# Kernel optimization log

Measured on AMD Instinct MI355X. Metric: run time of the kernel, lower is better.

The kernel has to match this reference:

```python
import jax, jax.numpy as jnp
import numpy as np

B, H, W, C = 16, 48, 48, 256
D_INNER = 2 * C          # ssm_ratio = 2.0
D_STATE = 1
DT_RANK = C // 16        # mamba convention: dt_rank = d_model // 16
HID = 4 * C              # mlp_ratio = 4.0
N = H * W


def _grid_neighbors(h, w):
    idx = np.arange(h * w).reshape(h, w)
    pad_r = -np.ones((1, w), np.int64)
    pad_c = -np.ones((h, 1), np.int64)
    up = np.concatenate([pad_r, idx[:-1]], 0)
    down = np.concatenate([idx[1:], pad_r], 0)
    left = np.concatenate([pad_c, idx[:, :-1]], 1)
    right = np.concatenate([idx[:, 1:], pad_c], 1)
    nb = np.stack([up, down, left, right], -1).reshape(h * w, 4)
    valid = nb >= 0
    return jnp.asarray(np.where(valid, nb, 0), np.int32), jnp.asarray(valid)

_NBR, _VALID = _grid_neighbors(H, W)


def _mst(x):
    """Input-adaptive MST (Prim) on the 4-connected pixel grid.
    Edge weight = exp(1 - cosine_similarity) between adjacent pixel features.
    Returns (order, par): Prim insertion order (a valid BFS-like topological order:
    every node's parent appears earlier) and parent node id per node."""
    b = x.shape[0]
    f = x.reshape(b, N, C)
    f = f / (jnp.linalg.norm(f, axis=-1, keepdims=True) + 1e-8)
    cos = jnp.einsum('bnc,bnkc->bnk', f, f[:, _NBR])          # (B,N,4)
    wgt = jnp.where(_VALID, jnp.exp(1.0 - cos), jnp.inf)

    def prim(wb):
        key = jnp.full((N,), jnp.inf, wb.dtype).at[0].set(0.0)
        par = jnp.zeros((N,), jnp.int32)
        intree = jnp.zeros((N,), bool)

        def step(carry, _):
            key, par, intree = carry
            u = jnp.argmin(jnp.where(intree, jnp.inf, key)).astype(jnp.int32)
            intree = intree.at[u].set(True)
            nb, wv = _NBR[u], wb[u]
            better = (~intree[nb]) & (wv < key[nb])
            key = key.at[nb].set(jnp.where(better, wv, key[nb]))
            par = par.at[nb].set(jnp.where(better, u, par[nb]))
            return (key, par, intree), u

        (_, par, _), order = jax.lax.scan(step, (key, par, intree), None, length=N)
        return order, par

    return jax.vmap(prim)(wgt)


def _ln(x, g, b):
    m = jnp.mean(x, -1, keepdims=True)
    v = jnp.var(x, -1, keepdims=True)
    return (x - m) * jax.lax.rsqrt(v + 1e-5) * g + b


def _tree_ssm(xn, order, par, W_in, b_in, W_xp, W_dt, b_dt, A_log, Dp, W_out, b_out):
    """Mamba-style selective scan generalized to a tree: the hidden state of node v
    recurses from its MST parent instead of the previous sequence position."""
    b = xn.shape[0]
    xf = xn.reshape(b, N, C)
    xz = xf @ W_in + b_in                               # (B,N,2*D_INNER)
    xi, z = xz[..., :D_INNER], xz[..., D_INNER:]
    xi = jax.nn.silu(xi)
    dbc = xi @ W_xp                                     # (B,N,DT_RANK+2)
    dtr = dbc[..., :DT_RANK]
    Bv = dbc[..., DT_RANK:DT_RANK + 1]                  # d_state = 1
    Cv = dbc[..., DT_RANK + 1:DT_RANK + 2]
    dt = jax.nn.softplus(dtr @ W_dt + b_dt)             # (B,N,D_INNER)
    A = -jnp.exp(A_log)                                 # (D_INNER,)
    decay = jnp.exp(dt * A)
    Bx = dt * Bv * xi

    def tree_scan(ob, pb, db, xb):
        def step(hbuf, v):
            hv = db[v] * hbuf[pb[v]] + xb[v]            # h[v] = decay*h[parent] + B*x
            return hbuf.at[v].set(hv), None
        hbuf, _ = jax.lax.scan(step, jnp.zeros((N, D_INNER), db.dtype), ob)
        return hbuf

    h = jax.vmap(tree_scan)(order, par, decay, Bx)      # (B,N,D_INNER)
    y = Cv * h + Dp * xi
    return ((y * jax.nn.silu(z)) @ W_out + b_out).reshape(xn.shape)


def setup_inputs():
    key = jax.random.key(0)
    ks = jax.random.split(key, 8)
    g = lambda k, shp, s=0.02: jax.random.normal(k, shp, jnp.float32) * s
    return {
        "x": jax.random.normal(ks[0], (B, H, W, C), jnp.float32),
        "norm1_w": jnp.ones((C,), jnp.float32), "norm1_b": jnp.zeros((C,), jnp.float32),
        "norm2_w": jnp.ones((C,), jnp.float32), "norm2_b": jnp.zeros((C,), jnp.float32),
        "W_in": g(ks[1], (C, 2 * D_INNER)), "b_in": jnp.zeros((2 * D_INNER,), jnp.float32),
        "W_xp": g(ks[2], (D_INNER, DT_RANK + 2 * D_STATE)),
        "W_dt": g(ks[3], (DT_RANK, D_INNER), 0.1), "b_dt": jnp.full((D_INNER,), -2.0, jnp.float32),
        "A_log": jnp.zeros((D_INNER,), jnp.float32), "Dp": jnp.ones((D_INNER,), jnp.float32),
        "W_out": g(ks[4], (D_INNER, C)), "b_out": jnp.zeros((C,), jnp.float32),
        "fc1_w": g(ks[5], (C, HID)), "fc1_b": jnp.zeros((HID,), jnp.float32),
        "fc2_w": g(ks[6], (HID, C)), "fc2_b": jnp.zeros((C,), jnp.float32),
    }


def reference(x, norm1_w, norm1_b, norm2_w, norm2_b, W_in, b_in, W_xp, W_dt, b_dt,
              A_log, Dp, W_out, b_out, fc1_w, fc1_b, fc2_w, fc2_b):
    order, par = _mst(jax.lax.stop_gradient(x))         # torch.no_grad() MST
    x = x + _tree_ssm(_ln(x, norm1_w, norm1_b), order, par,
                      W_in, b_in, W_xp, W_dt, b_dt, A_log, Dp, W_out, b_out)
    h = jax.nn.gelu(_ln(x, norm2_w, norm2_b) @ fc1_w + fc1_b, approximate=False)
    return x + h @ fc2_w + fc2_b
```

## Files before the change

kernel.cpp:

```cpp
#include <hip/hip_runtime.h>
#include <math.h>

#define NN 2304
#define BB 16
#define CC 256
#define DI 512
#define MM (BB*NN)

typedef __attribute__((ext_vector_type(8))) short bf16x8;
typedef __attribute__((ext_vector_type(4))) float f32x4;

__device__ inline unsigned short f2b(float f){
  unsigned u = __float_as_uint(f);
  u = u + 0x7FFFu + ((u>>16)&1u);
  return (unsigned short)(u>>16);
}
__device__ inline float b2f(unsigned short s){ return __uint_as_float(((unsigned)s)<<16); }
__device__ __forceinline__ int dstep(int d){ return (d==0)?-48:(d==1)?48:(d==2)?-1:1; }

__global__ __launch_bounds__(256) void k_prep(const float* __restrict__ W_in, const float* __restrict__ W_out,
    const float* __restrict__ fc1_w, const float* __restrict__ fc2_w, const float* __restrict__ W_xp,
    unsigned short* __restrict__ WinT, unsigned short* __restrict__ WoutT,
    unsigned short* __restrict__ fc1T, unsigned short* __restrict__ fc2T, float* __restrict__ WxpT)
{
  int idx = blockIdx.x*256 + threadIdx.x;
  if (idx < 262144){ int r=idx>>10, c=idx&1023; WinT[(size_t)c*256 + r] = f2b(W_in[idx]); return; }
  idx -= 262144;
  if (idx < 131072){ int r=idx>>8, c=idx&255; WoutT[(size_t)c*512 + r] = f2b(W_out[idx]); return; }
  idx -= 131072;
  if (idx < 262144){ int r=idx>>10, c=idx&1023; fc1T[(size_t)c*256 + r] = f2b(fc1_w[idx]); return; }
  idx -= 262144;
  if (idx < 262144){ int r=idx>>8, c=idx&255; fc2T[(size_t)c*1024 + r] = f2b(fc2_w[idx]); return; }
  idx -= 262144;
  if (idx < 9216){ int r=idx/18, c=idx-r*18; WxpT[(size_t)c*512 + r] = W_xp[idx]; }
}

__global__ __launch_bounds__(256) void k_normln(const float* __restrict__ xin, const float* __restrict__ g,
    const float* __restrict__ bta, float* __restrict__ innorm, unsigned short* __restrict__ outb)
{
  int row = blockIdx.x*4 + (threadIdx.x>>6); int lane=threadIdx.x&63;
  float4 v = *(const float4*)(xin + (size_t)row*CC + lane*4);
  float sq = v.x*v.x + v.y*v.y + v.z*v.z + v.w*v.w;
  float s  = v.x+v.y+v.z+v.w;
  #pragma unroll
  for (int o=32;o;o>>=1){ sq += __shfl_xor(sq,o); s += __shfl_xor(s,o); }
  if (lane==0) innorm[row] = 1.0f/(sqrtf(sq)+1e-8f);
  float m = s*(1.0f/256.0f);
  float dx=v.x-m, dy=v.y-m, dz=v.z-m, dw=v.w-m;
  float ss=dx*dx+dy*dy+dz*dz+dw*dw;
  #pragma unroll
  for (int o=32;o;o>>=1) ss += __shfl_xor(ss,o);
  float rs = rsqrtf(ss*(1.0f/256.0f)+1e-5f);
  int cb=lane*4;
  unsigned o0 = (unsigned)f2b(dx*rs*g[cb+0]+bta[cb+0]) | ((unsigned)f2b(dy*rs*g[cb+1]+bta[cb+1])<<16);
  unsigned o1 = (unsigned)f2b(dz*rs*g[cb+2]+bta[cb+2]) | ((unsigned)f2b(dw*rs*g[cb+3]+bta[cb+3])<<16);
  *(uint2*)(outb + (size_t)row*CC + cb) = make_uint2(o0,o1);
}

__global__ __launch_bounds__(256) void k_edge(const float* __restrict__ x, const float* __restrict__ innorm, float* __restrict__ wgt){
  int g = blockIdx.x*4 + (threadIdx.x>>6); int lane = threadIdx.x&63;
  int b = g/NN, n = g - b*NN;
  int r = n/48, c = n - (n/48)*48;
  const float* xb = x + ((size_t)b*NN)*CC;
  float4 vu = *(const float4*)(xb + (size_t)n*CC + lane*4);
  int nb0=(r>0)?n-48:-1, nb1=(r<47)?n+48:-1, nb2=(c>0)?n-1:-1, nb3=(c<47)?n+1:-1;
  float d0=0,d1=0,d2=0,d3=0;
  if (nb0>=0){ float4 t=*(const float4*)(xb+(size_t)nb0*CC+lane*4); d0=vu.x*t.x+vu.y*t.y+vu.z*t.z+vu.w*t.w; }
  if (nb1>=0){ float4 t=*(const float4*)(xb+(size_t)nb1*CC+lane*4); d1=vu.x*t.x+vu.y*t.y+vu.z*t.z+vu.w*t.w; }
  if (nb2>=0){ float4 t=*(const float4*)(xb+(size_t)nb2*CC+lane*4); d2=vu.x*t.x+vu.y*t.y+vu.z*t.z+vu.w*t.w; }
  if (nb3>=0){ float4 t=*(const float4*)(xb+(size_t)nb3*CC+lane*4); d3=vu.x*t.x+vu.y*t.y+vu.z*t.z+vu.w*t.w; }
  #pragma unroll
  for (int o=32;o;o>>=1){ d0+=__shfl_xor(d0,o); d1+=__shfl_xor(d1,o); d2+=__shfl_xor(d2,o); d3+=__shfl_xor(d3,o); }
  if (lane==0){
    float inu = innorm[g];
    float inf_ = __uint_as_float(0x7F800000u);
    float4 w;
    w.x = (nb0>=0)? expf(1.0f - d0*(inu*innorm[g-n+nb0])) : inf_;
    w.y = (nb1>=0)? expf(1.0f - d1*(inu*innorm[g-n+nb1])) : inf_;
    w.z = (nb2>=0)? expf(1.0f - d2*(inu*innorm[g-n+nb2])) : inf_;
    w.w = (nb3>=0)? expf(1.0f - d3*(inu*innorm[g-n+nb3])) : inf_;
    *(float4*)(wgt + (size_t)g*4) = w;
  }
}

#define INFB 0x7F800000u
#define NILA 0x3FFFu
__device__ void mst_body(unsigned char* smem, const float* __restrict__ wgt, int b,
    unsigned short* __restrict__ parpos_g, int* __restrict__ lvlorder,
    int* __restrict__ lvlstart, int* __restrict__ nlvl)
{
  unsigned* tmask = (unsigned*)smem;
  unsigned* pk    = (unsigned*)(smem + 9216);
  unsigned* comp   = pk;
  unsigned* bestw  = pk + 2304;
  unsigned* bestid = pk + 4608;
  unsigned short* par   = (unsigned short*)(smem + 46080);
  unsigned short* dpos  = (unsigned short*)(smem + 50688);
  int* hist = (int*)(smem + 55296);
  int* ctr  = (int*)(smem + 64512);
  const int tid = threadIdx.x;
  const float* wb = wgt + (size_t)b*NN*4;

  #pragma unroll
  for (int k=0;k<9;k++){ int v=tid+k*256; comp[v]=v; tmask[v]=0u; }
  __syncthreads();

  for (int round=0; round<14; round++){
    #pragma unroll
    for (int k=0;k<9;k++){ int v=tid+k*256; bestw[v]=INFB; bestid[v]=0xFFFFFFFFu; }
    __syncthreads();
    unsigned candw[9], candi[9];
    #pragma unroll
    for (int k=0;k<9;k++){
      int v=tid+k*256;
      unsigned cv=comp[v];
      int r=v/48, c=v-(v/48)*48;
      float4 w4 = *(const float4*)(wb + (size_t)v*4);
      unsigned cw=INFB, ci=0xFFFFFFFFu;
      if (r>0  && comp[v-48]!=cv){ unsigned wv=__float_as_uint(w4.x); if (wv<cw){cw=wv;ci=(unsigned)(v*4+0);} }
      if (r<47 && comp[v+48]!=cv){ unsigned wv=__float_as_uint(w4.y); if (wv<cw){cw=wv;ci=(unsigned)(v*4+1);} }
      if (c>0  && comp[v-1] !=cv){ unsigned wv=__float_as_uint(w4.z); if (wv<cw){cw=wv;ci=(unsigned)(v*4+2);} }
      if (c<47 && comp[v+1] !=cv){ unsigned wv=__float_as_uint(w4.w); if (wv<cw){cw=wv;ci=(unsigned)(v*4+3);} }
      candw[k]=cw; candi[k]=ci;
      if (cw!=INFB) atomicMin(&bestw[cv], cw);
    }
    __syncthreads();
    #pragma unroll
    for (int k=0;k<9;k++){
      if (candw[k]!=INFB){
        int v=tid+k*256; unsigned cv=comp[v];
        if (bestw[cv]==candw[k]) atomicMin(&bestid[cv], candi[k]);
      }
    }
    __syncthreads();
    unsigned hookS[9];
    int hooked = 0;
    #pragma unroll
    for (int k=0;k<9;k++){
      int v=tid+k*256; hookS[k]=0xFFFFFFFFu;
      if (comp[v]!=(unsigned)v) continue;
      unsigned id=bestid[v];
      if (id==0xFFFFFFFFu) continue;
      int u=(int)(id>>2), d=(int)(id&3);
      int o = u + dstep(d);
      unsigned s = comp[o];
      unsigned sid = bestid[s];
      bool mutual=false;
      if (sid!=0xFFFFFFFFu){
        int su=(int)(sid>>2), sd=(int)(sid&3);
        int so = su + dstep(sd);
        mutual = (comp[so]==(unsigned)v);
      }
      if (!mutual || (unsigned)v>s){ hookS[k]=s; hooked=1; }
    }
    __syncthreads();
    #pragma unroll
    for (int k=0;k<9;k++){
      if (hookS[k]==0xFFFFFFFFu) continue;
      int v=tid+k*256;
      unsigned id=bestid[v];
      int u=(int)(id>>2), d=(int)(id&3);
      int o = u + dstep(d);
      comp[v]=hookS[k];
      atomicOr(&tmask[u], 1u<<d);
      atomicOr(&tmask[o], 1u<<(d^1));
    }
    if (__syncthreads_count(hooked)==0) break;
    for (int it=0; it<16; it++){
      int ch=0;
      #pragma unroll
      for (int k=0;k<9;k++){
        int v=tid+k*256;
        unsigned c1=comp[v], c2=comp[c1];
        if (c1!=c2){ comp[v]=c2; ch=1; }
      }
      if (__syncthreads_count(ch)==0) break;
    }
  }
  __syncthreads();

  int a0;
  { unsigned m0 = tmask[0]; a0 = __ffs((int)(m0&0xFu))-1; }

  for (int pass=0; pass<2; pass++){
    for (int k=0;k<36;k++){
      int a = k*256+tid;
      int v = a>>2, d = a&3;
      unsigned mv = tmask[v];
      unsigned sc = NILA;
      unsigned vl = pass ? 8192u : 0u;
      if ((mv>>d)&1u){
        int w = v + dstep(d);
        unsigned mw = tmask[w];
        int rd = d^1;
        int nd = -1;
        #pragma unroll
        for (int kk=1;kk<=4;kk++){ int c2=(rd+kk)&3; if (nd<0 && ((mw>>c2)&1u)) nd=c2; }
        sc = (unsigned)(w*4+nd);
        if (sc==(unsigned)a0) sc=NILA;
        vl = pass ? (8192u + (((mv>>(4+d))&1u)? 1u : (unsigned)-1)) : 1u;
      }
      pk[a] = (sc<<14) | (vl & 0x3FFFu);
    }
    __syncthreads();
    for (int it=0; it<13; it++){
      unsigned stg[36];
      #pragma unroll
      for (int k=0;k<36;k++){
        int a=k*256+tid;
        unsigned mine=pk[a];
        unsigned s=mine>>14;
        if (s==NILA) stg[k]=mine;
        else {
          unsigned oth=pk[s];
          unsigned nv=(mine&0x3FFFu)+(oth&0x3FFFu);
          if (pass) nv -= 8192u;
          stg[k]=((oth>>14)<<14)|(nv&0x3FFFu);
        }
      }
      __syncthreads();
      #pragma unroll
      for (int k=0;k<36;k++) pk[k*256+tid]=stg[k];
      __syncthreads();
    }
    if (pass==0){
      for (int k=0;k<36;k++){
        int a=k*256+tid;
        int v=a>>2, d=a&3;
        if ((tmask[v]>>d)&1u){
          int w=v+dstep(d);
          int ra=w*4+(d^1);
          if ((pk[a]&0x3FFFu) > (pk[ra]&0x3FFFu)){
            atomicOr(&tmask[v], 16u<<d);
            par[w]=(unsigned short)v;
          }
        }
      }
      __syncthreads();
    }
  }
  if (tid==0){ par[0]=0; dpos[0]=0; ctr[3]=0; }
  __syncthreads();
  for (int k=0;k<36;k++){
    int a=k*256+tid;
    int v=a>>2, d=a&3;
    unsigned mv=tmask[v];
    if (((mv>>d)&1u) && ((mv>>(4+d))&1u)){
      int w=v+dstep(d);
      int S=(int)(pk[a]&0x3FFFu)-8192;
      int dep=1-S;
      dpos[w]=(unsigned short)dep;
      atomicMax(&ctr[3],dep);
    }
  }
  __syncthreads();
  int nlv_=ctr[3]+1;
  for (int i=tid;i<nlv_;i+=256) hist[i]=0;
  __syncthreads();
  for (int i=tid;i<NN;i+=256) atomicAdd(&hist[dpos[i]],1);
  __syncthreads();
  if (tid==0){
    int run=0;
    for (int l=0;l<nlv_;l++){ int c2=hist[l]; hist[l]=run; lvlstart[b*(NN+2)+l]=run; run+=c2; }
    lvlstart[b*(NN+2)+nlv_]=run;
    nlvl[b]=nlv_;
  }
  __syncthreads();
  for (int i=tid;i<NN;i+=256){
    int pos=atomicAdd(&hist[dpos[i]],1);
    lvlorder[b*NN+pos]=i;
    dpos[i]=(unsigned short)pos;
  }
  __syncthreads();
  for (int i=tid;i<NN;i+=256)
    parpos_g[b*NN + dpos[i]] = dpos[par[i]];
}

template<int EPI>
__device__ void gemm_body(unsigned short* lA, unsigned short* lB, int bm, int bn,
    const unsigned short* __restrict__ A, const unsigned short* __restrict__ BT,
    const float* __restrict__ bias, int Ndim, int K,
    const float* __restrict__ addin, float* __restrict__ fout,
    unsigned short* __restrict__ bout0, unsigned short* __restrict__ bout1,
    const int* __restrict__ lvl)
{
  int tid=threadIdx.x, wid=tid>>6, lane=tid&63;
  const unsigned short* Ab = A + (size_t)bm*128*K;
  const unsigned short* Bb = BT + (size_t)bn*128*K;
  int wr=wid>>1, wc=wid&1;
  f32x4 acc[4][4];
  #pragma unroll
  for (int m2=0;m2<4;m2++)
    #pragma unroll
    for (int n2=0;n2<4;n2++)
      #pragma unroll
      for (int j=0;j<4;j++) acc[m2][n2][j]=0.f;
  int r0 = tid>>2, c0 = (tid&3)*8;
  for (int k0=0;k0<K;k0+=32){
    int4 va0 = *(const int4*)(Ab + (size_t)r0*K + k0 + c0);
    int4 va1 = *(const int4*)(Ab + (size_t)(r0+64)*K + k0 + c0);
    int4 vb0 = *(const int4*)(Bb + (size_t)r0*K + k0 + c0);
    int4 vb1 = *(const int4*)(Bb + (size_t)(r0+64)*K + k0 + c0);
    __syncthreads();
    *(int4*)(lA + r0*32 + c0) = va0;
    *(int4*)(lA + (r0+64)*32 + c0) = va1;
    *(int4*)(lB + r0*32 + c0) = vb0;
    *(int4*)(lB + (r0+64)*32 + c0) = vb1;
    __syncthreads();
    int ra = (wr<<6) + (lane&15);
    int rb = (wc<<6) + (lane&15);
    int cb = (lane>>4)<<3;
    bf16x8 af[4], bfr[4];
    #pragma unroll
    for (int m2=0;m2<4;m2++) af[m2] = *(const bf16x8*)(lA + (ra+m2*16)*32 + cb);
    #pragma unroll
    for (int n2=0;n2<4;n2++) bfr[n2] = *(const bf16x8*)(lB + (rb+n2*16)*32 + cb);
    #pragma unroll
    for (int m2=0;m2<4;m2++)
      #pragma unroll
      for (int n2=0;n2<4;n2++)
        acc[m2][n2] = __builtin_amdgcn_mfma_f32_16x16x32_bf16(af[m2], bfr[n2], acc[m2][n2], 0,0,0);
  }
  int rr = (lane>>4)<<2, cc = lane&15;
  #pragma unroll
  for (int m2=0;m2<4;m2++){
    #pragma unroll
    for (int n2=0;n2<4;n2++){
      int col = (bn<<7) + (wc<<6) + (n2<<4) + cc;
      float bs = bias[col];
      #pragma unroll
      for (int j=0;j<4;j++){
        int row = (bm<<7) + (wr<<6) + (m2<<4) + rr + j;
        float v = acc[m2][n2][j] + bs;
        if (EPI==0){
          float sv = v * (1.0f/(1.0f+expf(-v)));
          if (col < DI) bout0[(size_t)row*DI + col] = f2b(sv);
          else          bout1[(size_t)row*DI + col - DI] = f2b(sv);
        } else if (EPI==1){
          size_t oi=(size_t)row*Ndim+col;
          fout[oi] = addin[oi] + v;
        } else if (EPI==2){
          size_t oi=(size_t)row*Ndim+col;
          bout0[oi] = f2b(0.5f*v*(1.0f+erff(v*0.70710678118f)));
        } else if (EPI==3){
          int grow = (row/NN)*NN + lvl[row];
          fout[(size_t)row*Ndim+col] = addin[(size_t)grow*Ndim+col] + v;
        } else {
          int grow = (row/NN)*NN + lvl[row];
          fout[(size_t)grow*Ndim+col] = addin[(size_t)row*Ndim+col] + v;
        }
      }
    }
  }
}

template<int EPI>
__global__ __launch_bounds__(256) void k_gemm(
    const unsigned short* __restrict__ A, const unsigned short* __restrict__ BT,
    const float* __restrict__ bias, int Ndim, int K,
    const float* __restrict__ addin, float* __restrict__ fout,
    unsigned short* __restrict__ bout0, unsigned short* __restrict__ bout1,
    const int* __restrict__ lvl)
{
  __shared__ __align__(16) unsigned short lAB[128*32*2];
  int ntn = Ndim>>7;
  int bm = blockIdx.x/ntn, bn = blockIdx.x - bm*ntn;
  gemm_body<EPI>(lAB, lAB+128*32, bm, bn, A, BT, bias, Ndim, K, addin, fout, bout0, bout1, lvl);
}

__global__ __launch_bounds__(256) void k_fused(
    const unsigned short* __restrict__ xn, const unsigned short* __restrict__ WinT,
    const float* __restrict__ b_in,
    unsigned short* __restrict__ xi_b, unsigned short* __restrict__ sz_b,
    const float* __restrict__ wgt, unsigned short* __restrict__ parpos_g,
    int* __restrict__ lvlorder, int* __restrict__ lvlstart, int* __restrict__ nlvl)
{
  __shared__ __align__(16) unsigned char smem[64528];
  if (blockIdx.x < BB){
    mst_body(smem, wgt, blockIdx.x, parpos_g, lvlorder, lvlstart, nlvl);
  } else {
    int bid = blockIdx.x - BB;
    int bm = bid>>3, bn = bid&7;
    gemm_body<0>((unsigned short*)smem, (unsigned short*)smem + 128*32, bm, bn,
                 xn, WinT, b_in, 1024, 256, nullptr, nullptr, xi_b, sz_b, nullptr);
  }
}

__global__ __launch_bounds__(256) void k_ln(const float* __restrict__ xin, const float* __restrict__ g,
    const float* __restrict__ bta, unsigned short* __restrict__ outb)
{
  int row = blockIdx.x*4 + (threadIdx.x>>6); int lane=threadIdx.x&63;
  float4 v = *(const float4*)(xin + (size_t)row*CC + lane*4);
  float s = v.x+v.y+v.z+v.w;
  #pragma unroll
  for (int o=32;o;o>>=1) s += __shfl_xor(s,o);
  float m = s*(1.0f/256.0f);
  float dx=v.x-m, dy=v.y-m, dz=v.z-m, dw=v.w-m;
  float ss=dx*dx+dy*dy+dz*dz+dw*dw;
  #pragma unroll
  for (int o=32;o;o>>=1) ss += __shfl_xor(ss,o);
  float rs = rsqrtf(ss*(1.0f/256.0f)+1e-5f);
  int cb=lane*4;
  unsigned o0 = (unsigned)f2b(dx*rs*g[cb+0]+bta[cb+0]) | ((unsigned)f2b(dy*rs*g[cb+1]+bta[cb+1])<<16);
  unsigned o1 = (unsigned)f2b(dz*rs*g[cb+2]+bta[cb+2]) | ((unsigned)f2b(dw*rs*g[cb+3]+bta[cb+3])<<16);
  *(uint2*)(outb + (size_t)row*CC + cb) = make_uint2(o0,o1);
}

__global__ __launch_bounds__(256) void k_dbc(const unsigned short* __restrict__ xi_b,
    const float* __restrict__ WxpT, float* __restrict__ dbc)
{
  int row = blockIdx.x*4 + (threadIdx.x>>6); int lane=threadIdx.x&63;
  int4 raw = *(const int4*)(xi_b + (size_t)row*DI + lane*8);
  float xf[8];
  xf[0]=b2f((unsigned short)((unsigned)raw.x&0xFFFFu)); xf[1]=b2f((unsigned short)((unsigned)raw.x>>16));
  xf[2]=b2f((unsigned short)((unsigned)raw.y&0xFFFFu)); xf[3]=b2f((unsigned short)((unsigned)raw.y>>16));
  xf[4]=b2f((unsigned short)((unsigned)raw.z&0xFFFFu)); xf[5]=b2f((unsigned short)((unsigned)raw.z>>16));
  xf[6]=b2f((unsigned short)((unsigned)raw.w&0xFFFFu)); xf[7]=b2f((unsigned short)((unsigned)raw.w>>16));
  for (int jc=0;jc<18;jc++){
    const float* wr_ = WxpT + (size_t)jc*DI + lane*8;
    float s=0.f;
    #pragma unroll
    for (int t=0;t<8;t++) s += xf[t]*wr_[t];
    #pragma unroll
    for (int o=32;o;o>>=1) s += __shfl_xor(s,o);
    if (lane==0) dbc[(size_t)row*18+jc]=s;
  }
}

__global__ __launch_bounds__(512) void k_dbx(const float* __restrict__ dbc, const unsigned short* __restrict__ xi_b,
  const float* __restrict__ W_dt, const float* __restrict__ b_dt, const float* __restrict__ A_log,
  const int* __restrict__ lvlorder,
  unsigned short* __restrict__ dec_cm, unsigned short* __restrict__ bx_cm)
{
  __shared__ int smap[32];
  __shared__ float sd[32][18];
  int c = threadIdx.x;
  int b = blockIdx.x/72, pg = blockIdx.x - b*72;
  int p0 = pg*32;
  if (c<32) smap[c] = b*NN + lvlorder[b*NN + p0 + c];
  __syncthreads();
  for (int i=c;i<32*18;i+=512){ int rr=i/18, q=i-rr*18; sd[rr][q]=dbc[(size_t)smap[rr]*18+q]; }
  __syncthreads();
  float wdt[16];
  #pragma unroll
  for (int r2=0;r2<16;r2++) wdt[r2]=W_dt[r2*DI+c];
  float bd=b_dt[c];
  float nA=-expf(A_log[c]);
  unsigned decp[16], bxp[16];
  #pragma unroll
  for (int rr=0;rr<32;rr++){
    float a=bd;
    #pragma unroll
    for (int r2=0;r2<16;r2++) a += sd[rr][r2]*wdt[r2];
    float dt = (a>20.f)? a : log1pf(expf(a));
    float dec = expf(dt*nA);
    float bx = dt*sd[rr][16]*b2f(xi_b[(size_t)smap[rr]*DI + c]);
    if (rr&1){ decp[rr>>1] |= ((unsigned)f2b(dec))<<16; bxp[rr>>1] |= ((unsigned)f2b(bx))<<16; }
    else     { decp[rr>>1]  =  (unsigned)f2b(dec);      bxp[rr>>1]  =  (unsigned)f2b(bx); }
  }
  size_t chb = ((size_t)b*DI + c)*NN + p0;
  uint4* dp = (uint4*)(dec_cm + chb);
  uint4* bp = (uint4*)(bx_cm + chb);
  #pragma unroll
  for (int q=0;q<4;q++){
    uint4 dv, bv;
    dv.x=decp[q*4+0]; dv.y=decp[q*4+1]; dv.z=decp[q*4+2]; dv.w=decp[q*4+3];
    bv.x=bxp[q*4+0];  bv.y=bxp[q*4+1];  bv.z=bxp[q*4+2];  bv.w=bxp[q*4+3];
    dp[q]=dv; bp[q]=bv;
  }
}

#define SCH 4
__global__ __launch_bounds__(256) void k_scan(const unsigned short* __restrict__ dec_cm,
    unsigned short* __restrict__ bx_cm,
    const unsigned short* __restrict__ parpos_g,
    const int* __restrict__ lvlstart, const int* __restrict__ nlvl)
{
  __shared__ unsigned short sdec[SCH*NN];
  __shared__ unsigned short sbx[SCH*NN];
  __shared__ unsigned short spp[NN];
  int b = blockIdx.x>>7, t = blockIdx.x&127;
  int c0 = t*SCH;
  int tid = threadIdx.x;
  const size_t gch = ((size_t)b*DI + c0)*NN;
  #pragma unroll
  for (int cc=0;cc<SCH;cc++){
    const uint2* gd = (const uint2*)(dec_cm + gch + (size_t)cc*NN);
    const uint2* gb = (const uint2*)(bx_cm + gch + (size_t)cc*NN);
    uint2* ld = (uint2*)(sdec + cc*NN);
    uint2* lb = (uint2*)(sbx + cc*NN);
    for (int i=tid;i<NN/4;i+=256){ ld[i]=gd[i]; lb[i]=gb[i]; }
  }
  for (int i=tid;i<NN;i+=256) spp[i]=parpos_g[b*NN+i];
  int nlv = nlvl[b];
  __syncthreads();
  for (int lvl=1; lvl<nlv; lvl++){
    int s=lvlstart[b*(NN+2)+lvl], e=lvlstart[b*(NN+2)+lvl+1];
    int tot=(e-s)*SCH;
    for (int idx=tid; idx<tot; idx+=256){
      int p = s + (idx>>2);
      int cc = idx&3;
      int pp = spp[p];
      float hv = b2f(sdec[cc*NN+p])*b2f(sbx[cc*NN+pp]) + b2f(sbx[cc*NN+p]);
      sbx[cc*NN+p] = f2b(hv);
    }
    __syncthreads();
  }
  #pragma unroll
  for (int cc=0;cc<SCH;cc++){
    uint2* gb = (uint2*)(bx_cm + gch + (size_t)cc*NN);
    const uint2* lb = (const uint2*)(sbx + cc*NN);
    for (int i=tid;i<NN/4;i+=256) gb[i]=lb[i];
  }
}

__global__ __launch_bounds__(512) void k_u(const unsigned short* __restrict__ h_cm,
    const unsigned short* __restrict__ xi_b, const unsigned short* __restrict__ sz_b,
    const float* __restrict__ dbc, const float* __restrict__ Dp,
    const int* __restrict__ lvlorder, unsigned short* __restrict__ u_perm)
{
  __shared__ int smap[32];
  __shared__ unsigned short hT[32*512];
  int c = threadIdx.x;
  int b = blockIdx.x/72, pg = blockIdx.x - b*72;
  int p0 = pg*32;
  if (c<32) smap[c] = b*NN + lvlorder[b*NN + p0 + c];
  {
    const uint4* gh = (const uint4*)(h_cm + ((size_t)b*DI + c)*NN + p0);
    #pragma unroll
    for (int q=0;q<4;q++){
      uint4 w = gh[q];
      unsigned ws[4] = {w.x,w.y,w.z,w.w};
      #pragma unroll
      for (int e=0;e<4;e++){
        hT[(q*8+e*2+0)*512 + c] = (unsigned short)(ws[e]&0xFFFFu);
        hT[(q*8+e*2+1)*512 + c] = (unsigned short)(ws[e]>>16);
      }
    }
  }
  float dpc = Dp[c];
  __syncthreads();
  #pragma unroll 4
  for (int rr=0;rr<32;rr++){
    int grow = smap[rr];
    float Cv = dbc[(size_t)grow*18+17];
    float xiv = b2f(xi_b[(size_t)grow*DI + c]);
    float szv = b2f(sz_b[(size_t)grow*DI + c]);
    float hv = b2f(hT[rr*512 + c]);
    float u = (Cv*hv + dpc*xiv)*szv;
    u_perm[((size_t)(b*NN + p0 + rr))*DI + c] = f2b(u);
  }
}

extern "C" void kernel_launch(void* const* d_in, const int* in_sizes, int n_in,
                              void* d_out, int out_size, void* d_ws, size_t ws_size,
                              hipStream_t stream) {
  (void)in_sizes; (void)n_in; (void)out_size; (void)ws_size;
  const float* x      = (const float*)d_in[0];
  const float* n1w    = (const float*)d_in[1];
  const float* n1b    = (const float*)d_in[2];
  const float* n2w    = (const float*)d_in[3];
  const float* n2b    = (const float*)d_in[4];
  const float* W_in   = (const float*)d_in[5];
  const float* b_in   = (const float*)d_in[6];
  const float* W_xp   = (const float*)d_in[7];
  const float* W_dt   = (const float*)d_in[8];
  const float* b_dt   = (const float*)d_in[9];
  const float* A_log  = (const float*)d_in[10];
  const float* Dp     = (const float*)d_in[11];
  const float* W_out  = (const float*)d_in[12];
  const float* b_out  = (const float*)d_in[13];
  const float* fc1_w  = (const float*)d_in[14];
  const float* fc1_b  = (const float*)d_in[15];
  const float* fc2_w  = (const float*)d_in[16];
  const float* fc2_b  = (const float*)d_in[17];

  char* base=(char*)d_ws; size_t off=0;
  auto alc=[&](size_t nb)->char*{ char* p=base+off; off=(off+nb+255)&~(size_t)255; return p; };
  float* wgt            = (float*)alc((size_t)MM*4*4);
  float* innorm         = (float*)alc((size_t)MM*4);
  unsigned short* parpos= (unsigned short*)alc((size_t)MM*2);
  int* lvlorder         = (int*)alc((size_t)MM*4);
  int* lvlstart         = (int*)alc((size_t)BB*(NN+2)*4);
  int* nlvl             = (int*)alc((size_t)BB*4);
  unsigned short* xi_b  = (unsigned short*)alc((size_t)MM*DI*2);
  unsigned short* sz_b  = (unsigned short*)alc((size_t)MM*DI*2);
  float* dbc            = (float*)alc((size_t)MM*18*4);
  unsigned short* dec_cm= (unsigned short*)alc((size_t)MM*DI*2);
  unsigned short* bx_cm = (unsigned short*)alc((size_t)MM*DI*2);
  unsigned short* WinT  = (unsigned short*)alc((size_t)CC*1024*2);
  unsigned short* WoutT = (unsigned short*)alc((size_t)DI*CC*2);
  unsigned short* fc1T  = (unsigned short*)alc((size_t)CC*1024*2);
  unsigned short* fc2T  = (unsigned short*)alc((size_t)1024*CC*2);
  float* WxpT           = (float*)alc((size_t)DI*18*4);
  unsigned short* xn      = (unsigned short*)dec_cm;
  unsigned short* h_cm    = bx_cm;
  unsigned short* u_perm  = dec_cm;
  float* x2_perm          = (float*)bx_cm;
  unsigned short* x2n_perm= dec_cm;
  unsigned short* g1_perm = xi_b;

  k_prep<<<dim3(3620),dim3(256),0,stream>>>(W_in, W_out, fc1_w, fc2_w, W_xp,
                                            WinT, WoutT, fc1T, fc2T, WxpT);
  k_normln<<<dim3(MM/4),dim3(256),0,stream>>>(x, n1w, n1b, innorm, xn);
  k_edge<<<dim3(MM/4),dim3(256),0,stream>>>(x, innorm, wgt);

  k_fused<<<dim3(BB + 288*8),dim3(256),0,stream>>>(xn, WinT, b_in, xi_b, sz_b,
                                                   wgt, parpos, lvlorder, lvlstart, nlvl);

  k_dbc<<<dim3(MM/4),dim3(256),0,stream>>>(xi_b, WxpT, dbc);
  k_dbx<<<dim3(MM/32),dim3(512),0,stream>>>(dbc, xi_b, W_dt, b_dt, A_log, lvlorder, dec_cm, bx_cm);
  k_scan<<<dim3(BB*128),dim3(256),0,stream>>>(dec_cm, bx_cm, parpos, lvlstart, nlvl);
  k_u<<<dim3(MM/32),dim3(512),0,stream>>>(h_cm, xi_b, sz_b, dbc, Dp, lvlorder, u_perm);

  k_gemm<3><<<dim3(288*2),dim3(256),0,stream>>>(u_perm, WoutT, b_out, 256, 512,
                                                x, x2_perm, nullptr, nullptr, lvlorder);
  k_ln<<<dim3(MM/4),dim3(256),0,stream>>>(x2_perm, n2w, n2b, x2n_perm);
  k_gemm<2><<<dim3(288*8),dim3(256),0,stream>>>(x2n_perm, fc1T, fc1_b, 1024, 256,
                                                nullptr, nullptr, g1_perm, nullptr, nullptr);
  k_gemm<4><<<dim3(288*2),dim3(256),0,stream>>>(g1_perm, fc2T, fc2_b, 256, 1024,
                                                x2_perm, (float*)d_out, nullptr, nullptr, lvlorder);
}
```

Before: 713.5 us.

## Merge weight prep into LN kernel, batch dbc reductions, single-wave tree scan

Folds the weight transpose/convert prep kernel into the first LayerNorm launch as extra blocks, removing one launch. In k_dbc, the 18 per-row dot products are computed first and then reduced together with interleaved shuffles instead of serially. In k_scan, level boundaries are cached in LDS and the level-by-level tree recurrence runs on a single 64-lane wave with wave barriers instead of block-wide __syncthreads, cutting synchronisation cost per level at the price of fewer threads doing per-level work.

```diff
diff --git a/kernel.cpp b/kernel.cpp
--- a/kernel.cpp
+++ b/kernel.cpp
@@ -18,26 +18,26 @@
 __device__ inline float b2f(unsigned short s){ return __uint_as_float(((unsigned)s)<<16); }
 __device__ __forceinline__ int dstep(int d){ return (d==0)?-48:(d==1)?48:(d==2)?-1:1; }
 
-__global__ __launch_bounds__(256) void k_prep(const float* __restrict__ W_in, const float* __restrict__ W_out,
+__global__ __launch_bounds__(256) void k_normln(const float* __restrict__ xin, const float* __restrict__ g,
+    const float* __restrict__ bta, float* __restrict__ innorm, unsigned short* __restrict__ outb,
+    const float* __restrict__ W_in, const float* __restrict__ W_out,
     const float* __restrict__ fc1_w, const float* __restrict__ fc2_w, const float* __restrict__ W_xp,
     unsigned short* __restrict__ WinT, unsigned short* __restrict__ WoutT,
     unsigned short* __restrict__ fc1T, unsigned short* __restrict__ fc2T, float* __restrict__ WxpT)
 {
-  int idx = blockIdx.x*256 + threadIdx.x;
-  if (idx < 262144){ int r=idx>>10, c=idx&1023; WinT[(size_t)c*256 + r] = f2b(W_in[idx]); return; }
-  idx -= 262144;
-  if (idx < 131072){ int r=idx>>8, c=idx&255; WoutT[(size_t)c*512 + r] = f2b(W_out[idx]); return; }
-  idx -= 131072;
-  if (idx < 262144){ int r=idx>>10, c=idx&1023; fc1T[(size_t)c*256 + r] = f2b(fc1_w[idx]); return; }
-  idx -= 262144;
-  if (idx < 262144){ int r=idx>>8, c=idx&255; fc2T[(size_t)c*1024 + r] = f2b(fc2_w[idx]); return; }
-  idx -= 262144;
-  if (idx < 9216){ int r=idx/18, c=idx-r*18; WxpT[(size_t)c*512 + r] = W_xp[idx]; }
-}
-
-__global__ __launch_bounds__(256) void k_normln(const float* __restrict__ xin, const float* __restrict__ g,
-    const float* __restrict__ bta, float* __restrict__ innorm, unsigned short* __restrict__ outb)
-{
+  if (blockIdx.x >= MM/4){
+    int idx = (blockIdx.x - MM/4)*256 + threadIdx.x;
+    if (idx < 262144){ int r=idx>>10, c=idx&1023; WinT[(size_t)c*256 + r] = f2b(W_in[idx]); return; }
+    idx -= 262144;
+    if (idx < 131072){ int r=idx>>8, c=idx&255; WoutT[(size_t)c*512 + r] = f2b(W_out[idx]); return; }
+    idx -= 131072;
+    if (idx < 262144){ int r=idx>>10, c=idx&1023; fc1T[(size_t)c*256 + r] = f2b(fc1_w[idx]); return; }
+    idx -= 262144;
+    if (idx < 262144){ int r=idx>>8, c=idx&255; fc2T[(size_t)c*1024 + r] = f2b(fc2_w[idx]); return; }
+    idx -= 262144;
+    if (idx < 9216){ int r=idx/18, c=idx-r*18; WxpT[(size_t)c*512 + r] = W_xp[idx]; }
+    return;
+  }
   int row = blockIdx.x*4 + (threadIdx.x>>6); int lane=threadIdx.x&63;
   float4 v = *(const float4*)(xin + (size_t)row*CC + lane*4);
   float sq = v.x*v.x + v.y*v.y + v.z*v.z + v.w*v.w;
@@ -416,15 +416,23 @@
   xf[2]=b2f((unsigned short)((unsigned)raw.y&0xFFFFu)); xf[3]=b2f((unsigned short)((unsigned)raw.y>>16));
   xf[4]=b2f((unsigned short)((unsigned)raw.z&0xFFFFu)); xf[5]=b2f((unsigned short)((unsigned)raw.z>>16));
   xf[6]=b2f((unsigned short)((unsigned)raw.w&0xFFFFu)); xf[7]=b2f((unsigned short)((unsigned)raw.w>>16));
+  float s[18];
+  #pragma unroll
   for (int jc=0;jc<18;jc++){
     const float* wr_ = WxpT + (size_t)jc*DI + lane*8;
-    float s=0.f;
-    #pragma unroll
-    for (int t=0;t<8;t++) s += xf[t]*wr_[t];
-    #pragma unroll
-    for (int o=32;o;o>>=1) s += __shfl_xor(s,o);
-    if (lane==0) dbc[(size_t)row*18+jc]=s;
-  }
+    float t=0.f;
+    #pragma unroll
+    for (int q=0;q<8;q++) t += xf[q]*wr_[q];
+    s[jc]=t;
+  }
+  #pragma unroll
+  for (int o=32;o;o>>=1){
+    #pragma unroll
+    for (int jc=0;jc<18;jc++) s[jc] += __shfl_xor(s[jc],o);
+  }
+  #pragma unroll
+  for (int jc=0;jc<18;jc++)
+    if (lane==jc) dbc[(size_t)row*18+jc]=s[jc];
 }
 
 __global__ __launch_bounds__(512) void k_dbx(const float* __restrict__ dbc, const unsigned short* __restrict__ xi_b,
@@ -479,6 +487,7 @@
   __shared__ unsigned short sdec[SCH*NN];
   __shared__ unsigned short sbx[SCH*NN];
   __shared__ unsigned short spp[NN];
+  __shared__ int slvl[NN+2];
   int b = blockIdx.x>>7, t = blockIdx.x&127;
   int c0 = t*SCH;
   int tid = threadIdx.x;
@@ -493,19 +502,27 @@
   }
   for (int i=tid;i<NN;i+=256) spp[i]=parpos_g[b*NN+i];
   int nlv = nlvl[b];
-  __syncthreads();
-  for (int lvl=1; lvl<nlv; lvl++){
-    int s=lvlstart[b*(NN+2)+lvl], e=lvlstart[b*(NN+2)+lvl+1];
-    int tot=(e-s)*SCH;
-    for (int idx=tid; idx<tot; idx+=256){
-      int p = s + (idx>>2);
-      int cc = idx&3;
-      int pp = spp[p];
-      float hv = b2f(sdec[cc*NN+p])*b2f(sbx[cc*NN+pp]) + b2f(sbx[cc*NN+p]);
-      sbx[cc*NN+p] = f2b(hv);
-    }
-    __syncthreads();
-  }
+  for (int i=tid;i<=nlv;i+=256) slvl[i]=lvlstart[b*(NN+2)+i];
+  __syncthreads();
+  if (tid < 64){
+    volatile unsigned short* vbx = sbx;
+    int s = slvl[1];
+    for (int lvl=1; lvl<nlv; lvl++){
+      int e = slvl[lvl+1];
+      int tot=(e-s)*SCH;
+      for (int idx=tid; idx<tot; idx+=64){
+        int p = s + (idx>>2);
+        int cc = idx&3;
+        int pp = spp[p];
+        float hv = b2f(sdec[cc*NN+p])*b2f(vbx[cc*NN+pp]) + b2f(vbx[cc*NN+p]);
+        vbx[cc*NN+p] = f2b(hv);
+      }
+      s = e;
+      __builtin_amdgcn_wave_barrier();
+      __builtin_amdgcn_sched_barrier(0);
+    }
+  }
+  __syncthreads();
   #pragma unroll
   for (int cc=0;cc<SCH;cc++){
     uint2* gb = (uint2*)(bx_cm + gch + (size_t)cc*NN);
@@ -600,9 +617,9 @@
   unsigned short* x2n_perm= dec_cm;
   unsigned short* g1_perm = xi_b;
 
-  k_prep<<<dim3(3620),dim3(256),0,stream>>>(W_in, W_out, fc1_w, fc2_w, W_xp,
-                                            WinT, WoutT, fc1T, fc2T, WxpT);
-  k_normln<<<dim3(MM/4),dim3(256),0,stream>>>(x, n1w, n1b, innorm, xn);
+  k_normln<<<dim3(MM/4 + 3620),dim3(256),0,stream>>>(x, n1w, n1b, innorm, xn,
+                                                     W_in, W_out, fc1_w, fc2_w, W_xp,
+                                                     WinT, WoutT, fc1T, fc2T, WxpT);
   k_edge<<<dim3(MM/4),dim3(256),0,stream>>>(x, innorm, wgt);
 
   k_fused<<<dim3(BB + 288*8),dim3(256),0,stream>>>(xn, WinT, b_in, xi_b, sz_b,
```

New measurement: 762.2 us. +6.8%, slower.
